# Kernel optimization log

Hardware: AMD Instinct MI355X
Metric: run time of the kernel (lower is better)

The kernel has to match this reference:

```python
import jax, jax.numpy as jnp
import numpy as np

B = 16384
D = 128
N_LAYER = 2
USER_NUM, ITEM_NUM, ENTITY_NUM = 100000, 50000, 50000
H1, H2 = 256, 128  # hidden_layers


def setup_inputs() -> dict:
    key = jax.random.key(0)
    ks = jax.random.split(key, 20)
    inp = {
        'user_ids': jax.random.randint(ks[0], (B,), 0, USER_NUM),
        'item_ids': jax.random.randint(ks[1], (B,), 0, ITEM_NUM),
        'rec_target': jax.random.uniform(ks[2], (B,), dtype=jnp.float32),
        # embedding tables
        'user_tbl': jax.random.normal(ks[3], (USER_NUM, D), dtype=jnp.float32) * 0.02,
        'item_tbl': jax.random.normal(ks[4], (ITEM_NUM, D), dtype=jnp.float32) * 0.02,
        'entity_tbl': jax.random.normal(ks[5], (ENTITY_NUM, D), dtype=jnp.float32) * 0.02,
        # cross-compress weights (torch.rand -> uniform)
        'w_vv': jax.random.uniform(ks[6], (D, 1), dtype=jnp.float32),
        'w_ev': jax.random.uniform(ks[7], (D, 1), dtype=jnp.float32),
        'w_ve': jax.random.uniform(ks[8], (D, 1), dtype=jnp.float32),
        'w_ee': jax.random.uniform(ks[9], (D, 1), dtype=jnp.float32),
        'bias_v': jax.random.uniform(ks[10], (1,), dtype=jnp.float32),
        'bias_e': jax.random.uniform(ks[11], (1,), dtype=jnp.float32),
        # user low MLP (Linear D->D)
        'Wu': jax.random.normal(ks[12], (D, D), dtype=jnp.float32) * 0.05,
        'bu': jnp.zeros((D,), dtype=jnp.float32),
        # rec MLP: 2D -> H1 -> H2 -> 1
        'W1': jax.random.normal(ks[13], (2 * D, H1), dtype=jnp.float32) * 0.05,
        'b1': jnp.zeros((H1,), dtype=jnp.float32),
        'W2': jax.random.normal(ks[14], (H1, H2), dtype=jnp.float32) * 0.05,
        'b2': jnp.zeros((H2,), dtype=jnp.float32),
        'W3': jax.random.normal(ks[15], (H2, 1), dtype=jnp.float32) * 0.05,
        'b3': jnp.zeros((1,), dtype=jnp.float32),
    }
    return inp


def _cross_compress(item, head, w_vv, w_ev, w_ve, w_ee, bias_v, bias_e):
    # c[b,i,j] = item[b,i]*head[b,j]; c_t[b,i,j] = head[b,i]*item[b,j]
    # (c @ w)[b,i] = item[b,i] * (head @ w)[b]; (c_t @ w)[b,i] = head[b,i] * (item @ w)[b]
    hv = head @ w_vv  # [B,1]
    iv = item @ w_ev  # [B,1]
    he = head @ w_ve  # [B,1]
    ie = item @ w_ee  # [B,1]
    item_c = item * hv + head * iv + bias_v
    head_c = item * he + head * ie + bias_e
    return item_c, head_c


def reference(user_ids, item_ids, rec_target, user_tbl, item_tbl, entity_tbl,
              w_vv, w_ev, w_ve, w_ee, bias_v, bias_e,
              Wu, bu, W1, b1, W2, b2, W3, b3):
    # train_type == 'rec' branch
    user_embed = user_tbl[user_ids]      # [B, D]
    item_embed = item_tbl[item_ids]      # [B, D]
    head_embed = entity_tbl[item_ids]    # [B, D]
    for _ in range(N_LAYER):
        user_embed = jax.nn.relu(user_embed @ Wu + bu)  # linear_layer (dropout=identity at eval)
        item_embed, head_embed = _cross_compress(
            item_embed, head_embed, w_vv, w_ev, w_ve, w_ee, bias_v, bias_e)
    high = jnp.concatenate([user_embed, item_embed], axis=1)  # [B, 2D]
    h = jax.nn.relu(high @ W1 + b1)
    h = jax.nn.relu(h @ W2 + b2)
    rec_out = jax.nn.relu(h @ W3 + b3)  # [B, 1]
    return rec_out[:, 0], rec_target
```

## Files before the change

### kernel.cpp

```cpp
#include <hip/hip_runtime.h>

#define BATCH 16384
#define DIM 128
#define STRIDE 264

typedef __attribute__((ext_vector_type(8))) short short8;
typedef __attribute__((ext_vector_type(4))) float floatx4;

__device__ __forceinline__ ushort f2bf(float f) {
    union { float f; uint u; } c; c.f = f;
    return (ushort)((c.u + 0x7FFFu + ((c.u >> 16) & 1u)) >> 16);
}
__device__ __forceinline__ float bf2f(ushort h) {
    union { uint u; float f; } c; c.u = ((uint)h) << 16;
    return c.f;
}
__device__ __forceinline__ ushort4 f4_to_bf4(float4 v) {
    return make_ushort4(f2bf(v.x), f2bf(v.y), f2bf(v.z), f2bf(v.w));
}

__global__ __launch_bounds__(256) void convert_kernel(
    const float* __restrict__ Wu, const float* __restrict__ W1,
    const float* __restrict__ W2, ushort* __restrict__ Wut,
    ushort* __restrict__ W1t, ushort* __restrict__ W2t)
{
    __shared__ float s[64][65];
    const int b = blockIdx.x;
    const float* W; ushort* Wt; int K, N, tk, tn;
    if (b < 4)       { W = Wu; Wt = Wut; K = 128; N = 128; tk = b >> 1;        tn = b & 1; }
    else if (b < 20) { W = W1; Wt = W1t; K = 256; N = 256; tk = (b - 4) >> 2;  tn = (b - 4) & 3; }
    else             { W = W2; Wt = W2t; K = 256; N = 128; tk = (b - 20) >> 1; tn = (b - 20) & 1; }
    const int k0 = tk * 64, n0 = tn * 64;
    const int tx = threadIdx.x & 63, ty = threadIdx.x >> 6;
    #pragma unroll
    for (int i = 0; i < 16; ++i) {
        int r = i * 4 + ty;
        s[r][tx] = W[(size_t)(k0 + r) * N + n0 + tx];
    }
    __syncthreads();
    const int p = threadIdx.x & 31, nb = threadIdx.x >> 5;
    #pragma unroll
    for (int i = 0; i < 8; ++i) {
        int n = i * 8 + nb;
        uint v = (uint)f2bf(s[2 * p][n]) | ((uint)f2bf(s[2 * p + 1][n]) << 16);
        ((uint*)Wt)[(((size_t)(n0 + n) * K + k0) >> 1) + p] = v;
    }
}

template<int K, int N>
__device__ __forceinline__ void layer_mfma(
    const ushort* __restrict__ src, const ushort* __restrict__ Wt,
    const float* __restrict__ bias, ushort* __restrict__ dst, int tid)
{
    const int wave = tid >> 6, lane = tid & 63;
    const int n15 = lane & 15, quad = lane >> 4;
    constexpr int NT = N / 16, KF = K / 32;
    for (int nt = wave; nt < NT; nt += 4) {
        const int n0 = nt * 16;
        short8 bfr[KF];
        const ushort* wrow = Wt + (size_t)(n0 + n15) * K + quad * 8;
        #pragma unroll
        for (int kf = 0; kf < KF; ++kf)
            bfr[kf] = *(const short8*)(wrow + kf * 32);
        const float b = bias[n0 + n15];
        #pragma unroll
        for (int mt = 0; mt < 2; ++mt) {
            floatx4 acc = {0.f, 0.f, 0.f, 0.f};
            const ushort* arow = src + (mt * 16 + n15) * STRIDE + quad * 8;
            #pragma unroll
            for (int kf = 0; kf < KF; ++kf) {
                short8 afr = *(const short8*)(arow + kf * 32);
                acc = __builtin_amdgcn_mfma_f32_16x16x32_bf16(afr, bfr[kf], acc, 0, 0, 0);
            }
            ushort* drow = dst + (mt * 16 + quad * 4) * STRIDE + n0 + n15;
            #pragma unroll
            for (int r = 0; r < 4; ++r)
                drow[r * STRIDE] = f2bf(fmaxf(acc[r] + b, 0.f));
        }
    }
}

__global__ __launch_bounds__(256) void fused_kernel(
    const int* __restrict__ user_ids, const int* __restrict__ item_ids,
    const float* __restrict__ rec_target,
    const float* __restrict__ user_tbl, const float* __restrict__ item_tbl,
    const float* __restrict__ entity_tbl,
    const float* __restrict__ w_vv, const float* __restrict__ w_ev,
    const float* __restrict__ w_ve, const float* __restrict__ w_ee,
    const float* __restrict__ bias_v, const float* __restrict__ bias_e,
    const ushort* __restrict__ Wut, const float* __restrict__ bu,
    const ushort* __restrict__ W1t, const float* __restrict__ b1,
    const ushort* __restrict__ W2t, const float* __restrict__ b2,
    const float* __restrict__ W3, const float* __restrict__ b3,
    float* __restrict__ out)
{
    __shared__ ushort bufA[32 * STRIDE];
    __shared__ ushort bufB[32 * STRIDE];
    const int r0  = blockIdx.x * 32;
    const int tid = threadIdx.x;
    const int row = tid >> 3, l = tid & 7;

    if (tid < 32) out[BATCH + r0 + tid] = rec_target[r0 + tid];

    {
        const int uid = user_ids[r0 + row];
        const float4* src = (const float4*)(user_tbl + (size_t)uid * DIM + l * 16);
        ushort* dst = &bufA[row * STRIDE + l * 16];
        #pragma unroll
        for (int i = 0; i < 4; ++i)
            *(ushort4*)&dst[i * 4] = f4_to_bf4(src[i]);
    }

    {
        const int id = item_ids[r0 + row];
        const float4* ip = (const float4*)(item_tbl   + (size_t)id * DIM + l * 16);
        const float4* hp = (const float4*)(entity_tbl + (size_t)id * DIM + l * 16);
        float4 it4[4], hd4[4];
        #pragma unroll
        for (int i = 0; i < 4; ++i) { it4[i] = ip[i]; hd4[i] = hp[i]; }
        const float bv = bias_v[0], be = bias_e[0];
        #pragma unroll
        for (int lay = 0; lay < 2; ++lay) {
            float hv = 0.f, iv = 0.f, he = 0.f, ie = 0.f;
            #pragma unroll
            for (int i = 0; i < 4; ++i) {
                float4 wvv = ((const float4*)w_vv)[l * 4 + i];
                float4 wev = ((const float4*)w_ev)[l * 4 + i];
                float4 wve = ((const float4*)w_ve)[l * 4 + i];
                float4 wee = ((const float4*)w_ee)[l * 4 + i];
                hv += hd4[i].x * wvv.x + hd4[i].y * wvv.y + hd4[i].z * wvv.z + hd4[i].w * wvv.w;
                iv += it4[i].x * wev.x + it4[i].y * wev.y + it4[i].z * wev.z + it4[i].w * wev.w;
                he += hd4[i].x * wve.x + hd4[i].y * wve.y + hd4[i].z * wve.z + hd4[i].w * wve.w;
                ie += it4[i].x * wee.x + it4[i].y * wee.y + it4[i].z * wee.z + it4[i].w * wee.w;
            }
            hv += __shfl_xor(hv, 1); hv += __shfl_xor(hv, 2); hv += __shfl_xor(hv, 4);
            iv += __shfl_xor(iv, 1); iv += __shfl_xor(iv, 2); iv += __shfl_xor(iv, 4);
            he += __shfl_xor(he, 1); he += __shfl_xor(he, 2); he += __shfl_xor(he, 4);
            ie += __shfl_xor(ie, 1); ie += __shfl_xor(ie, 2); ie += __shfl_xor(ie, 4);
            #pragma unroll
            for (int i = 0; i < 4; ++i) {
                float4 t = it4[i], h = hd4[i];
                it4[i].x = t.x * hv + h.x * iv + bv;  hd4[i].x = t.x * he + h.x * ie + be;
                it4[i].y = t.y * hv + h.y * iv + bv;  hd4[i].y = t.y * he + h.y * ie + be;
                it4[i].z = t.z * hv + h.z * iv + bv;  hd4[i].z = t.z * he + h.z * ie + be;
                it4[i].w = t.w * hv + h.w * iv + bv;  hd4[i].w = t.w * he + h.w * ie + be;
            }
        }
        ushort* dst = &bufA[row * STRIDE + 128 + l * 16];
        #pragma unroll
        for (int i = 0; i < 4; ++i)
            *(ushort4*)&dst[i * 4] = f4_to_bf4(it4[i]);
    }
    __syncthreads();

    layer_mfma<128, 128>(bufA, Wut, bu, bufB, tid);
    __syncthreads();
    layer_mfma<128, 128>(bufB, Wut, bu, bufA, tid);
    __syncthreads();
    layer_mfma<256, 256>(bufA, W1t, b1, bufB, tid);
    __syncthreads();
    layer_mfma<256, 128>(bufB, W2t, b2, bufA, tid);
    __syncthreads();

    {
        const ushort* h2 = &bufA[row * STRIDE + l * 16];
        float p = 0.f;
        #pragma unroll
        for (int i = 0; i < 4; ++i) {
            ushort4 h4 = *(const ushort4*)&h2[i * 4];
            float4 w = ((const float4*)W3)[l * 4 + i];
            p += bf2f(h4.x) * w.x + bf2f(h4.y) * w.y + bf2f(h4.z) * w.z + bf2f(h4.w) * w.w;
        }
        p += __shfl_xor(p, 1); p += __shfl_xor(p, 2); p += __shfl_xor(p, 4);
        if (l == 0) out[r0 + row] = fmaxf(p + b3[0], 0.f);
    }
}

extern "C" void kernel_launch(void* const* d_in, const int* in_sizes, int n_in,
                              void* d_out, int out_size, void* d_ws, size_t ws_size,
                              hipStream_t stream)
{
    const int*   user_ids   = (const int*)  d_in[0];
    const int*   item_ids   = (const int*)  d_in[1];
    const float* rec_target = (const float*)d_in[2];
    const float* user_tbl   = (const float*)d_in[3];
    const float* item_tbl   = (const float*)d_in[4];
    const float* entity_tbl = (const float*)d_in[5];
    const float* w_vv       = (const float*)d_in[6];
    const float* w_ev       = (const float*)d_in[7];
    const float* w_ve       = (const float*)d_in[8];
    const float* w_ee       = (const float*)d_in[9];
    const float* bias_v     = (const float*)d_in[10];
    const float* bias_e     = (const float*)d_in[11];
    const float* Wu         = (const float*)d_in[12];
    const float* bu         = (const float*)d_in[13];
    const float* W1         = (const float*)d_in[14];
    const float* b1         = (const float*)d_in[15];
    const float* W2         = (const float*)d_in[16];
    const float* b2         = (const float*)d_in[17];
    const float* W3         = (const float*)d_in[18];
    const float* b3         = (const float*)d_in[19];
    float* out = (float*)d_out;

    ushort* Wut = (ushort*)d_ws;
    ushort* W1t = Wut + 128 * 128;
    ushort* W2t = W1t + 256 * 256;

    convert_kernel<<<28, 256, 0, stream>>>(Wu, W1, W2, Wut, W1t, W2t);
    fused_kernel<<<BATCH / 32, 256, 0, stream>>>(
        user_ids, item_ids, rec_target, user_tbl, item_tbl, entity_tbl,
        w_vv, w_ev, w_ve, w_ee, bias_v, bias_e,
        Wut, bu, W1t, b1, W2t, b2, W3, b3, out);
}
```

Before: 168.1 us.

## Store activations and weights in MFMA fragment-native layout

Weights are pre-packed by the conversion kernel into per-lane short8 MFMA fragments, so each lane loads its B operand with one coalesced 16-byte read. Activations in shared memory are kept in the same fragment-tiled layout, so A fragments load as contiguous short8 per lane and are hoisted into registers once per layer instead of being reloaded for every output tile. The epilogue scatters results straight into the next layer's fragment layout, and separate buffers replace the two ping-pong arrays. The cost is more register pressure from holding A fragments, 16-bit scattered LDS stores, and possible bank conflicts in the new layout.

```diff
diff --git a/kernel.cpp b/kernel.cpp
--- a/kernel.cpp
+++ b/kernel.cpp
@@ -2,7 +2,6 @@
 
 #define BATCH 16384
 #define DIM 128
-#define STRIDE 264
 
 typedef __attribute__((ext_vector_type(8))) short short8;
 typedef __attribute__((ext_vector_type(4))) float floatx4;
@@ -19,63 +18,63 @@
     return make_ushort4(f2bf(v.x), f2bf(v.y), f2bf(v.z), f2bf(v.w));
 }
 
+__device__ __forceinline__ int slot_idx(int KT, int m, int k) {
+    return (((m >> 4) * KT + (k >> 5)) << 6) + (((k >> 3) & 3) << 4) + (m & 15);
+}
+
 __global__ __launch_bounds__(256) void convert_kernel(
     const float* __restrict__ Wu, const float* __restrict__ W1,
-    const float* __restrict__ W2, ushort* __restrict__ Wut,
-    ushort* __restrict__ W1t, ushort* __restrict__ W2t)
-{
-    __shared__ float s[64][65];
-    const int b = blockIdx.x;
-    const float* W; ushort* Wt; int K, N, tk, tn;
-    if (b < 4)       { W = Wu; Wt = Wut; K = 128; N = 128; tk = b >> 1;        tn = b & 1; }
-    else if (b < 20) { W = W1; Wt = W1t; K = 256; N = 256; tk = (b - 4) >> 2;  tn = (b - 4) & 3; }
-    else             { W = W2; Wt = W2t; K = 256; N = 128; tk = (b - 20) >> 1; tn = (b - 20) & 1; }
-    const int k0 = tk * 64, n0 = tn * 64;
-    const int tx = threadIdx.x & 63, ty = threadIdx.x >> 6;
+    const float* __restrict__ W2, short8* __restrict__ WF)
+{
+    const int f    = blockIdx.x * 4 + (threadIdx.x >> 6);
+    const int lane = threadIdx.x & 63;
+    const int q = lane >> 4, r = lane & 15;
+    const float* W; int N, nt, kf, fl; short8* dst;
+    if (f < 32)       { W = Wu; N = 128; fl = f;       nt = fl >> 2; kf = fl & 3; dst = WF;         }
+    else if (f < 160) { W = W1; N = 256; fl = f - 32;  nt = fl >> 3; kf = fl & 7; dst = WF + 2048;  }
+    else              { W = W2; N = 128; fl = f - 160; nt = fl >> 3; kf = fl & 7; dst = WF + 10240; }
+    const int n = nt * 16 + r, k0 = kf * 32 + q * 8;
+    short8 v;
     #pragma unroll
-    for (int i = 0; i < 16; ++i) {
-        int r = i * 4 + ty;
-        s[r][tx] = W[(size_t)(k0 + r) * N + n0 + tx];
-    }
-    __syncthreads();
-    const int p = threadIdx.x & 31, nb = threadIdx.x >> 5;
+    for (int j = 0; j < 8; ++j)
+        v[j] = (short)f2bf(W[(size_t)(k0 + j) * N + n]);
+    dst[fl * 64 + lane] = v;
+}
+
+template<int KF, int NT, int DKT>
+__device__ __forceinline__ void layer_mfma(
+    const short8* __restrict__ src, const short8* __restrict__ WF,
+    const float* __restrict__ bias, ushort* __restrict__ dst, int tid)
+{
+    const int wave = tid >> 6, lane = tid & 63;
+    const int q = lane >> 4, r = lane & 15;
+    short8 a[2][KF];
     #pragma unroll
-    for (int i = 0; i < 8; ++i) {
-        int n = i * 8 + nb;
-        uint v = (uint)f2bf(s[2 * p][n]) | ((uint)f2bf(s[2 * p + 1][n]) << 16);
-        ((uint*)Wt)[(((size_t)(n0 + n) * K + k0) >> 1) + p] = v;
-    }
-}
-
-template<int K, int N>
-__device__ __forceinline__ void layer_mfma(
-    const ushort* __restrict__ src, const ushort* __restrict__ Wt,
-    const float* __restrict__ bias, ushort* __restrict__ dst, int tid)
-{
-    const int wave = tid >> 6, lane = tid & 63;
-    const int n15 = lane & 15, quad = lane >> 4;
-    constexpr int NT = N / 16, KF = K / 32;
+    for (int mt = 0; mt < 2; ++mt)
+        #pragma unroll
+        for (int kf = 0; kf < KF; ++kf)
+            a[mt][kf] = src[(mt * KF + kf) * 64 + lane];
+    #pragma unroll
     for (int nt = wave; nt < NT; nt += 4) {
-        const int n0 = nt * 16;
-        short8 bfr[KF];
-        const ushort* wrow = Wt + (size_t)(n0 + n15) * K + quad * 8;
+        const int col = nt * 16 + r;
+        short8 b[KF];
         #pragma unroll
         for (int kf = 0; kf < KF; ++kf)
-            bfr[kf] = *(const short8*)(wrow + kf * 32);
-        const float b = bias[n0 + n15];
+            b[kf] = WF[(nt * KF + kf) * 64 + lane];
+        const float bs = bias[col];
+        const int kc = col >> 5, qc = (col >> 3) & 3, e = col & 7;
         #pragma unroll
         for (int mt = 0; mt < 2; ++mt) {
             floatx4 acc = {0.f, 0.f, 0.f, 0.f};
-            const ushort* arow = src + (mt * 16 + n15) * STRIDE + quad * 8;
-            #pragma unroll
-            for (int kf = 0; kf < KF; ++kf) {
-                short8 afr = *(const short8*)(arow + kf * 32);
-                acc = __builtin_amdgcn_mfma_f32_16x16x32_bf16(afr, bfr[kf], acc, 0, 0, 0);
+            #pragma unroll
+            for (int kf = 0; kf < KF; ++kf)
+                acc = __builtin_amdgcn_mfma_f32_16x16x32_bf16(a[mt][kf], b[kf], acc, 0, 0, 0);
+            #pragma unroll
+            for (int rr = 0; rr < 4; ++rr) {
+                const int rlow = q * 4 + rr;
+                dst[(size_t)((((mt * DKT + kc) << 6) + (qc << 4) + rlow) * 8 + e)] =
+                    f2bf(fmaxf(acc[rr] + bs, 0.f));
             }
-            ushort* drow = dst + (mt * 16 + quad * 4) * STRIDE + n0 + n15;
-            #pragma unroll
-            for (int r = 0; r < 4; ++r)
-                drow[r * STRIDE] = f2bf(fmaxf(acc[r] + b, 0.f));
         }
     }
 }
@@ -88,14 +87,17 @@
     const float* __restrict__ w_vv, const float* __restrict__ w_ev,
     const float* __restrict__ w_ve, const float* __restrict__ w_ee,
     const float* __restrict__ bias_v, const float* __restrict__ bias_e,
-    const ushort* __restrict__ Wut, const float* __restrict__ bu,
-    const ushort* __restrict__ W1t, const float* __restrict__ b1,
-    const ushort* __restrict__ W2t, const float* __restrict__ b2,
+    const short8* __restrict__ WF, const float* __restrict__ bu,
+    const float* __restrict__ b1, const float* __restrict__ b2,
     const float* __restrict__ W3, const float* __restrict__ b3,
     float* __restrict__ out)
 {
-    __shared__ ushort bufA[32 * STRIDE];
-    __shared__ ushort bufB[32 * STRIDE];
+    __shared__ short8 sU0[512];
+    __shared__ short8 sU1[512];
+    __shared__ short8 sHI[1024];
+    __shared__ short8 sH1[1024];
+    __shared__ short8 sH2[512];
+
     const int r0  = blockIdx.x * 32;
     const int tid = threadIdx.x;
     const int row = tid >> 3, l = tid & 7;
@@ -105,10 +107,12 @@
     {
         const int uid = user_ids[r0 + row];
         const float4* src = (const float4*)(user_tbl + (size_t)uid * DIM + l * 16);
-        ushort* dst = &bufA[row * STRIDE + l * 16];
-        #pragma unroll
-        for (int i = 0; i < 4; ++i)
-            *(ushort4*)&dst[i * 4] = f4_to_bf4(src[i]);
+        ushort* p = (ushort*)sU0;
+        #pragma unroll
+        for (int i = 0; i < 4; ++i) {
+            const int col = l * 16 + i * 4;
+            *(ushort4*)&p[slot_idx(4, row, col) * 8 + (col & 7)] = f4_to_bf4(src[i]);
+        }
     }
 
     {
@@ -146,30 +150,36 @@
                 it4[i].w = t.w * hv + h.w * iv + bv;  hd4[i].w = t.w * he + h.w * ie + be;
             }
         }
-        ushort* dst = &bufA[row * STRIDE + 128 + l * 16];
-        #pragma unroll
-        for (int i = 0; i < 4; ++i)
-            *(ushort4*)&dst[i * 4] = f4_to_bf4(it4[i]);
-    }
-    __syncthreads();
-
-    layer_mfma<128, 128>(bufA, Wut, bu, bufB, tid);
-    __syncthreads();
-    layer_mfma<128, 128>(bufB, Wut, bu, bufA, tid);
-    __syncthreads();
-    layer_mfma<256, 256>(bufA, W1t, b1, bufB, tid);
-    __syncthreads();
-    layer_mfma<256, 128>(bufB, W2t, b2, bufA, tid);
+        ushort* p = (ushort*)sHI;
+        #pragma unroll
+        for (int i = 0; i < 4; ++i) {
+            const int col = 128 + l * 16 + i * 4;
+            *(ushort4*)&p[slot_idx(8, row, col) * 8 + (col & 7)] = f4_to_bf4(it4[i]);
+        }
+    }
+    __syncthreads();
+
+    layer_mfma<4, 8, 4>(sU0, WF,          bu, (ushort*)sU1, tid);
+    __syncthreads();
+    layer_mfma<4, 8, 8>(sU1, WF,          bu, (ushort*)sHI, tid);
+    __syncthreads();
+    layer_mfma<8, 16, 8>(sHI, WF + 2048,  b1, (ushort*)sH1, tid);
+    __syncthreads();
+    layer_mfma<8, 8, 4>(sH1, WF + 10240,  b2, (ushort*)sH2, tid);
     __syncthreads();
 
     {
-        const ushort* h2 = &bufA[row * STRIDE + l * 16];
         float p = 0.f;
         #pragma unroll
-        for (int i = 0; i < 4; ++i) {
-            ushort4 h4 = *(const ushort4*)&h2[i * 4];
-            float4 w = ((const float4*)W3)[l * 4 + i];
-            p += bf2f(h4.x) * w.x + bf2f(h4.y) * w.y + bf2f(h4.z) * w.z + bf2f(h4.w) * w.w;
+        for (int i = 0; i < 2; ++i) {
+            const int c8 = l * 2 + i;
+            short8 h = sH2[(((row >> 4) * 4 + (c8 >> 2)) << 6) + ((c8 & 3) << 4) + (row & 15)];
+            float4 w0 = ((const float4*)W3)[c8 * 2];
+            float4 w1 = ((const float4*)W3)[c8 * 2 + 1];
+            p += bf2f((ushort)h[0]) * w0.x + bf2f((ushort)h[1]) * w0.y
+               + bf2f((ushort)h[2]) * w0.z + bf2f((ushort)h[3]) * w0.w
+               + bf2f((ushort)h[4]) * w1.x + bf2f((ushort)h[5]) * w1.y
+               + bf2f((ushort)h[6]) * w1.z + bf2f((ushort)h[7]) * w1.w;
         }
         p += __shfl_xor(p, 1); p += __shfl_xor(p, 2); p += __shfl_xor(p, 4);
         if (l == 0) out[r0 + row] = fmaxf(p + b3[0], 0.f);
@@ -202,13 +212,11 @@
     const float* b3         = (const float*)d_in[19];
     float* out = (float*)d_out;
 
-    ushort* Wut = (ushort*)d_ws;
-    ushort* W1t = Wut + 128 * 128;
-    ushort* W2t = W1t + 256 * 256;
-
-    convert_kernel<<<28, 256, 0, stream>>>(Wu, W1, W2, Wut, W1t, W2t);
+    short8* WF = (short8*)d_ws;
+
+    convert_kernel<<<56, 256, 0, stream>>>(Wu, W1, W2, WF);
     fused_kernel<<<BATCH / 32, 256, 0, stream>>>(
         user_ids, item_ids, rec_target, user_tbl, item_tbl, entity_tbl,
         w_vv, w_ev, w_ve, w_ee, bias_v, bias_e,
-        Wut, bu, W1t, b1, W2t, b2, W3, b3, out);
-}
+        WF, bu, b1, b2, W3, b3, out);
+}
```

Result: faster. 155.9 us (-7.3%).
